# Kernel optimization log

Measured on AMD Instinct MI355X. Metric: run time of the kernel, lower is better.

Reference implementation:

```python
import jax, jax.numpy as jnp
import numpy as np

C = 256      # d_model
H = 8        # nhead
DF = 1024    # dim_feedforward
LE = 2048    # ego tokens
LA = 2048    # other-agent tokens
N_MATCH = 1024


def setup_inputs() -> dict:
    key = jax.random.key(0)
    ks = jax.random.split(key, 16)
    def rn(k, shape, s=0.02):
        return jax.random.normal(k, shape, dtype=jnp.float32) * s
    inp = {}
    inp['x_ego'] = jax.random.normal(ks[0], (LE, C), dtype=jnp.float32)
    inp['x_agent'] = jax.random.normal(ks[1], (LA, C), dtype=jnp.float32)
    # query_fusion MLP(2C -> C -> C -> C), torch Linear weight is (out, in)
    inp['Wf1'] = rn(ks[2], (C, 2 * C)); inp['bf1'] = jnp.zeros((C,), jnp.float32)
    inp['Wf2'] = rn(ks[3], (C, C));     inp['bf2'] = jnp.zeros((C,), jnp.float32)
    inp['Wf3'] = rn(ks[4], (C, C));     inp['bf3'] = jnp.zeros((C,), jnp.float32)
    # nn.MultiheadAttention packed in-proj and out-proj
    inp['Wqkv'] = rn(ks[5], (3 * C, C)); inp['bqkv'] = jnp.zeros((3 * C,), jnp.float32)
    inp['Wo'] = rn(ks[6], (C, C));       inp['bo'] = jnp.zeros((C,), jnp.float32)
    # FFN
    inp['W1'] = rn(ks[7], (DF, C)); inp['b1'] = jnp.zeros((DF,), jnp.float32)
    inp['W2'] = rn(ks[8], (C, DF)); inp['b2'] = jnp.zeros((C,), jnp.float32)
    # LayerNorms
    inp['g1'] = jnp.ones((C,), jnp.float32); inp['be1'] = jnp.zeros((C,), jnp.float32)
    inp['g2'] = jnp.ones((C,), jnp.float32); inp['be2'] = jnp.zeros((C,), jnp.float32)
    # unique 1D positions: first N_MATCH agent positions overlap ego, rest don't
    inp['pos_ego'] = jnp.arange(LE, dtype=jnp.int32)
    pa = np.concatenate([np.arange(N_MATCH), np.arange(LA - N_MATCH) + 10_000_000])
    inp['pos_agent'] = jnp.asarray(pa, dtype=jnp.int32)
    inp['n_remain'] = LA - N_MATCH  # static python int
    return inp


def _ln(t, g, b):
    m = t.mean(-1, keepdims=True)
    v = t.var(-1, keepdims=True)
    return (t - m) / jnp.sqrt(v + 1e-5) * g + b


def reference(x_ego, x_agent, Wf1, bf1, Wf2, bf2, Wf3, bf3, Wqkv, bqkv, Wo, bo,
              W1, b1, W2, b2, g1, be1, g2, be2, pos_ego, pos_agent, n_remain):
    # ---- position-keyed grouping / fuse (replaces the host-side dict loop) ----
    eq = pos_agent[:, None] == pos_ego[None, :]          # [La, Le]
    matched_e = eq.any(axis=0)                           # ego token has same-pos agent token
    agent_for_ego = jnp.argmax(eq, axis=0)               # [Le] matching agent index (valid where matched)
    fused_in = jnp.concatenate([x_ego, x_agent[agent_for_ego]], axis=-1)  # [Le, 2C]
    h = jax.nn.relu(fused_in @ Wf1.T + bf1)
    h = jax.nn.relu(h @ Wf2.T + bf2)
    fused = h @ Wf3.T + bf3                              # query_fusion MLP output [Le, C]
    ego_out = jnp.where(matched_e[:, None], fused, x_ego)
    # agent tokens with no ego match, in original agent order (fixed count n_remain)
    remain_idx = jnp.nonzero(~eq.any(axis=1), size=n_remain)[0]
    q = jnp.concatenate([ego_out, x_agent[remain_idx]], axis=0)[None]  # (1, Lq, C)
    kv = jnp.concatenate([x_ego, x_agent], axis=0)[None]               # (1, Lk, C)
    # ---- MultiheadAttention (batch_first, eval: dropout off) ----
    Wq, Wk, Wv = jnp.split(Wqkv, 3, axis=0)
    bq, bk, bv = jnp.split(bqkv, 3, axis=0)
    dh = C // H
    def heads(t, W, b):
        return (t @ W.T + b).reshape(1, -1, H, dh).transpose(0, 2, 1, 3)
    qh, kh, vh = heads(q, Wq, bq), heads(kv, Wk, bk), heads(kv, Wv, bv)
    scores = jnp.einsum('bhqd,bhkd->bhqk', qh, kh) / (float(dh) ** 0.5)
    attn = jax.nn.softmax(scores, axis=-1)
    o = jnp.einsum('bhqk,bhkd->bhqd', attn, vh).transpose(0, 2, 1, 3).reshape(1, -1, C)
    o = o @ Wo.T + bo
    # ---- residual + norm1 + FFN + residual + norm2 ----
    yq = _ln(q + o, g1, be1)
    ff = jax.nn.relu(yq @ W1.T + b1) @ W2.T + b2
    return _ln(yq + ff, g2, be2)
```

## Files before the change

### kernel.cpp

```cpp
#include <hip/hip_runtime.h>


#define LE 2048
#define LA 2048
#define CDIM 256
#define HN 8
#define DH 32
#define DFF 1024
#define NREM 1024
#define LQC 3072
#define LKC 4096
#define KSPLIT 4
#define NIT (LKC / KSPLIT / 64)

typedef unsigned short u16;
typedef unsigned int u32;
typedef __attribute__((ext_vector_type(8))) short bf16x8;
typedef __attribute__((ext_vector_type(4))) float f32x4;

__device__ __forceinline__ u32 pk_bf16(float a, float b) {
    u32 ua = (__builtin_bit_cast(u32, a) + 0x8000u) >> 16;
    u32 ub = (__builtin_bit_cast(u32, b) + 0x8000u) >> 16;
    return ua | (ub << 16);
}
__device__ __forceinline__ u16 bf16_1(float a) {
    return (u16)((__builtin_bit_cast(u32, a) + 0x8000u) >> 16);
}
__device__ __forceinline__ float fast_exp2(float x) {
    return __builtin_amdgcn_exp2f(x);
}

__global__ __launch_bounds__(1024) void k_match(const int* __restrict__ pos_ego,
                                                const int* __restrict__ pos_agent,
                                                int* __restrict__ afe,
                                                int* __restrict__ matched,
                                                int* __restrict__ unmatched) {
    __shared__ int keyA[4096], valA[4096], keyE[4096];
    const int t = threadIdx.x;
#pragma unroll
    for (int i = 0; i < 4; ++i) { keyA[t + i * 1024] = -1; keyE[t + i * 1024] = -1; }
    __syncthreads();
#pragma unroll
    for (int i = 0; i < 2; ++i) {
        int a = t + i * 1024;
        int p = pos_agent[a];
        u32 h = ((u32)p * 2654435761u) >> 20;
        while (true) {
            int prev = atomicCAS(&keyA[h], -1, p);
            if (prev == -1) { valA[h] = a; break; }
            h = (h + 1) & 4095;
        }
        int e = t + i * 1024;
        int pe = pos_ego[e];
        u32 he = ((u32)pe * 2654435761u) >> 20;
        while (true) {
            int prev = atomicCAS(&keyE[he], -1, pe);
            if (prev == -1) break;
            he = (he + 1) & 4095;
        }
    }
    __syncthreads();
#pragma unroll
    for (int i = 0; i < 2; ++i) {
        int e = t + i * 1024;
        int p = pos_ego[e];
        u32 h = ((u32)p * 2654435761u) >> 20;
        int idx = 0, fnd = 0;
        while (true) {
            int k = keyA[h];
            if (k == p) { idx = valA[h]; fnd = 1; break; }
            if (k == -1) break;
            h = (h + 1) & 4095;
        }
        afe[e] = idx;
        matched[e] = fnd;
        int a = t + i * 1024;
        int pa_ = pos_agent[a];
        u32 ha = ((u32)pa_ * 2654435761u) >> 20;
        int fnd2 = 0;
        while (true) {
            int k = keyE[ha];
            if (k == pa_) { fnd2 = 1; break; }
            if (k == -1) break;
            ha = (ha + 1) & 4095;
        }
        unmatched[a] = !fnd2;
    }
}

__global__ __launch_bounds__(256) void k_prep(const float* __restrict__ x_ego,
                                              const float* __restrict__ x_agent,
                                              u16* __restrict__ kv_b) {
    int t = blockIdx.x * 256 + threadIdx.x;
    int j = t >> 5, c8 = t & 31;
    const float* src = (j < LE) ? (x_ego + (size_t)j * CDIM)
                                : (x_agent + (size_t)(j - LE) * CDIM);
    float4 f0 = *(const float4*)(src + c8 * 8);
    float4 f1 = *(const float4*)(src + c8 * 8 + 4);
    uint4 o;
    o.x = pk_bf16(f0.x, f0.y); o.y = pk_bf16(f0.z, f0.w);
    o.z = pk_bf16(f1.x, f1.y); o.w = pk_bf16(f1.z, f1.w);
    *(uint4*)(kv_b + (size_t)j * CDIM + c8 * 8) = o;
}

struct WPtrs { const float* p[7]; };
__constant__ __device__ const int woff[8] = {0, 131072, 196608, 262144,
                                             458752, 524288, 786432, 1048576};

__global__ __launch_bounds__(256) void k_stage2(const int* __restrict__ unmatched,
                                                int* __restrict__ remain,
                                                const int* __restrict__ afe,
                                                const float* __restrict__ x_ego,
                                                const float* __restrict__ x_agent,
                                                u16* __restrict__ fused_b,
                                                WPtrs wp, u16* __restrict__ wb) {
    int b = blockIdx.x;
    if (b == 0) {
        __shared__ int s[256];
        int t = threadIdx.x;
        int base_i = t * 8;
        int flags[8];
        int cnt = 0;
#pragma unroll
        for (int j = 0; j < 8; ++j) { flags[j] = unmatched[base_i + j]; cnt += flags[j]; }
        s[t] = cnt;
        __syncthreads();
        for (int off = 1; off < 256; off <<= 1) {
            int v = (t >= off) ? s[t - off] : 0;
            __syncthreads();
            s[t] += v;
            __syncthreads();
        }
        int pos = s[t] - cnt;
#pragma unroll
        for (int j = 0; j < 8; ++j) {
            if (flags[j]) {
                if (pos < NREM) remain[pos] = base_i + j;
                pos++;
            }
        }
    } else if (b <= 512) {
        int t = (b - 1) * 256 + threadIdx.x;
        int e = t >> 6, c8 = t & 63;
        const float* src;
        int col;
        if (c8 < 32) { src = x_ego + (size_t)e * CDIM; col = c8 * 8; }
        else { src = x_agent + (size_t)afe[e] * CDIM; col = (c8 - 32) * 8; }
        float4 f0 = *(const float4*)(src + col);
        float4 f1 = *(const float4*)(src + col + 4);
        uint4 o;
        o.x = pk_bf16(f0.x, f0.y); o.y = pk_bf16(f0.z, f0.w);
        o.z = pk_bf16(f1.x, f1.y); o.w = pk_bf16(f1.z, f1.w);
        *(uint4*)(fused_b + (size_t)e * 512 + c8 * 8) = o;
    } else {
        int g = ((b - 513) * 256 + threadIdx.x) * 8;
        int s = 0;
#pragma unroll
        for (int i = 1; i < 7; ++i) s += (g >= woff[i]);
        const float* src = wp.p[s] + (g - woff[s]);
        float4 f0 = *(const float4*)(src);
        float4 f1 = *(const float4*)(src + 4);
        uint4 o;
        o.x = pk_bf16(f0.x, f0.y); o.y = pk_bf16(f0.z, f0.w);
        o.z = pk_bf16(f1.x, f1.y); o.w = pk_bf16(f1.z, f1.w);
        *(uint4*)(wb + g) = o;
    }
}

__global__ __launch_bounds__(256) void k_finalize_q(const int* __restrict__ matched,
                                                    const int* __restrict__ remain,
                                                    const float* __restrict__ x_ego,
                                                    const float* __restrict__ x_agent,
                                                    float* __restrict__ qbuf,
                                                    u16* __restrict__ qbuf_b) {
    int t = blockIdx.x * 256 + threadIdx.x;
    int row = t >> 5, c8 = t & 31;
    const float* src;
    if (row < LE) {
        src = matched[row] ? (qbuf + (size_t)row * CDIM) : (x_ego + (size_t)row * CDIM);
    } else {
        int idx = remain[row - LE];
        idx = min(max(idx, 0), LA - 1);
        src = x_agent + (size_t)idx * CDIM;
    }
    float4 f0 = *(const float4*)(src + c8 * 8);
    float4 f1 = *(const float4*)(src + c8 * 8 + 4);
    float* dst = qbuf + (size_t)row * CDIM + c8 * 8;
    *(float4*)(dst) = f0;
    *(float4*)(dst + 4) = f1;
    uint4 o;
    o.x = pk_bf16(f0.x, f0.y); o.y = pk_bf16(f0.z, f0.w);
    o.z = pk_bf16(f1.x, f1.y); o.w = pk_bf16(f1.z, f1.w);
    *(uint4*)(qbuf_b + (size_t)row * CDIM + c8 * 8) = o;
}

template <int EPI, bool RELU>
__global__ __launch_bounds__(256) void gemm_bf16(const u16* __restrict__ A,
                                                 const u16* __restrict__ B,
                                                 const float* __restrict__ bias,
                                                 void* __restrict__ C,
                                                 int M, int N, int K) {
    const int tid = threadIdx.x;
    const int w = tid >> 6, lane = tid & 63;
    const int quad = lane >> 4, qi = lane & 15;
    const int wm = w >> 1, wn = w & 1;
    const int bm = blockIdx.y * 64, bn = blockIdx.x * 64;

    const u16* pa0 = A + (size_t)(bm + wm * 32 + qi) * K + quad * 8;
    const u16* pa1 = pa0 + (size_t)16 * K;
    const u16* pb0 = B + (size_t)(bn + wn * 32 + qi) * K + quad * 8;
    const u16* pb1 = pb0 + (size_t)16 * K;

    f32x4 acc00 = {0.f, 0.f, 0.f, 0.f}, acc01 = {0.f, 0.f, 0.f, 0.f};
    f32x4 acc10 = {0.f, 0.f, 0.f, 0.f}, acc11 = {0.f, 0.f, 0.f, 0.f};

#pragma unroll 4
    for (int k = 0; k < K; k += 32) {
        bf16x8 a0 = *(const bf16x8*)(pa0 + k);
        bf16x8 a1 = *(const bf16x8*)(pa1 + k);
        bf16x8 b0 = *(const bf16x8*)(pb0 + k);
        bf16x8 b1 = *(const bf16x8*)(pb1 + k);
        acc00 = __builtin_amdgcn_mfma_f32_16x16x32_bf16(a0, b0, acc00, 0, 0, 0);
        acc01 = __builtin_amdgcn_mfma_f32_16x16x32_bf16(a0, b1, acc01, 0, 0, 0);
        acc10 = __builtin_amdgcn_mfma_f32_16x16x32_bf16(a1, b0, acc10, 0, 0, 0);
        acc11 = __builtin_amdgcn_mfma_f32_16x16x32_bf16(a1, b1, acc11, 0, 0, 0);
    }

#pragma unroll
    for (int i = 0; i < 2; ++i) {
#pragma unroll
        for (int j = 0; j < 2; ++j) {
            f32x4 acc = (i == 0) ? (j == 0 ? acc00 : acc01) : (j == 0 ? acc10 : acc11);
            int n = bn + wn * 32 + j * 16 + qi;
            int mbase = bm + wm * 32 + i * 16 + quad * 4;
            float bs = bias[n];
            float v[4];
#pragma unroll
            for (int r = 0; r < 4; ++r) {
                float x = acc[r] + bs;
                if (RELU) x = fmaxf(x, 0.f);
                v[r] = x;
            }
            if (EPI == 0) {
                float* Cf = (float*)C;
#pragma unroll
                for (int r = 0; r < 4; ++r) Cf[(size_t)(mbase + r) * N + n] = v[r];
            } else {
                u16* Cb = (u16*)C;
#pragma unroll
                for (int r = 0; r < 4; ++r) Cb[(size_t)(mbase + r) * N + n] = bf16_1(v[r]);
            }
        }
    }
}

__global__ __launch_bounds__(256) void k_qkv(const u16* __restrict__ qbuf_b,
                                             const u16* __restrict__ kv_b,
                                             const u16* __restrict__ Wq,
                                             const u16* __restrict__ Wkv,
                                             const float* __restrict__ bqkv,
                                             u16* __restrict__ qb,
                                             u16* __restrict__ kbp,
                                             u16* __restrict__ vtb,
                                             float qscale) {
    int b = blockIdx.x;
    const u16 *A, *B;
    const float* bias;
    int bm, bn, mode;
    if (b < 192) {
        A = qbuf_b; B = Wq; bias = bqkv;
        bm = (b >> 2) * 64; bn = (b & 3) * 64; mode = 0;
    } else {
        int c = b - 192;
        A = kv_b; B = Wkv; bias = bqkv + 256;
        bm = (c >> 3) * 64; bn = (c & 7) * 64; mode = 1;
    }
    const int tid = threadIdx.x;
    const int w = tid >> 6, lane = tid & 63;
    const int quad = lane >> 4, qi = lane & 15;
    const int wm = w >> 1, wn = w & 1;
    const int K = 256;

    const u16* pa0 = A + (size_t)(bm + wm * 32 + qi) * K + quad * 8;
    const u16* pa1 = pa0 + (size_t)16 * K;
    const u16* pb0 = B + (size_t)(bn + wn * 32 + qi) * K + quad * 8;
    const u16* pb1 = pb0 + (size_t)16 * K;

    f32x4 acc00 = {0.f, 0.f, 0.f, 0.f}, acc01 = {0.f, 0.f, 0.f, 0.f};
    f32x4 acc10 = {0.f, 0.f, 0.f, 0.f}, acc11 = {0.f, 0.f, 0.f, 0.f};
#pragma unroll 4
    for (int k = 0; k < 256; k += 32) {
        bf16x8 a0 = *(const bf16x8*)(pa0 + k);
        bf16x8 a1 = *(const bf16x8*)(pa1 + k);
        bf16x8 b0 = *(const bf16x8*)(pb0 + k);
        bf16x8 b1 = *(const bf16x8*)(pb1 + k);
        acc00 = __builtin_amdgcn_mfma_f32_16x16x32_bf16(a0, b0, acc00, 0, 0, 0);
        acc01 = __builtin_amdgcn_mfma_f32_16x16x32_bf16(a0, b1, acc01, 0, 0, 0);
        acc10 = __builtin_amdgcn_mfma_f32_16x16x32_bf16(a1, b0, acc10, 0, 0, 0);
        acc11 = __builtin_amdgcn_mfma_f32_16x16x32_bf16(a1, b1, acc11, 0, 0, 0);
    }
#pragma unroll
    for (int i = 0; i < 2; ++i) {
#pragma unroll
        for (int j = 0; j < 2; ++j) {
            f32x4 acc = (i == 0) ? (j == 0 ? acc00 : acc01) : (j == 0 ? acc10 : acc11);
            int n = bn + wn * 32 + j * 16 + qi;
            int mbase = bm + wm * 32 + i * 16 + quad * 4;
            float bs = bias[n];
            float v[4];
#pragma unroll
            for (int r = 0; r < 4; ++r) v[r] = acc[r] + bs;
            if (mode == 0) {
#pragma unroll
                for (int r = 0; r < 4; ++r)
                    qb[(size_t)(mbase + r) * 256 + n] = bf16_1(v[r] * qscale);
            } else if (n < 256) {
#pragma unroll
                for (int r = 0; r < 4; ++r)
                    kbp[(size_t)(mbase + r) * 256 + n] = bf16_1(v[r]);
            } else {
                ushort4 o4;
                o4.x = bf16_1(v[0]); o4.y = bf16_1(v[1]);
                o4.z = bf16_1(v[2]); o4.w = bf16_1(v[3]);
                *(ushort4*)(vtb + (size_t)(n - 256) * LKC + mbase) = o4;
            }
        }
    }
}

__global__ __launch_bounds__(256) void attn_mfma(const u16* __restrict__ qb,
                                                 const u16* __restrict__ kb,
                                                 const u16* __restrict__ vtb,
                                                 float* __restrict__ Pl,
                                                 float* __restrict__ Pacc) {
    __shared__ u16 Kt[2][64 * 32];
    __shared__ u16 Vt[2][32 * 64];
    __shared__ u16 plds[4][16 * 64];
    const int tid = threadIdx.x;
    const int w = tid >> 6, lane = tid & 63;
    const int quad = lane >> 4, qi = lane & 15;
    const int h = blockIdx.y, ks = blockIdx.z;
    const int q0 = blockIdx.x * 64 + w * 16;

    bf16x8 qf = *(const bf16x8*)(qb + (size_t)(q0 + qi) * CDIM + h * DH + quad * 8);

    f32x4 O0 = {0.f, 0.f, 0.f, 0.f}, O1 = {0.f, 0.f, 0.f, 0.f};
    float lsum = 0.f;

    const int krow = w * 16 + (lane >> 2), kcp = lane & 3;
    const int kc = kcp ^ (krow & 3);
    const u16* kg0 = kb + (size_t)krow * CDIM + h * DH + kc * 8;
    const int kdst = krow * 32 + kcp * 8;
    const int vd = w * 8 + (lane >> 3), vcp = lane & 7;
    const int vc = vcp ^ (vd & 7);
    const u16* vg0 = vtb + (size_t)(h * DH + vd) * LKC + vc * 8;
    const int vdst = vd * 64 + vcp * 8;

    const int ka0 = qi * 32 + ((quad ^ (qi & 3)) << 3);
    const int v00o = qi * 64 + ((quad ^ (qi & 7)) << 3);
    const int v01o = qi * 64 + (((quad + 4) ^ (qi & 7)) << 3);
    const int swz = (qi & 7);
    const int rd0 = qi * 64 + ((quad ^ swz) << 3);
    const int rd1 = qi * 64 + (((4 + quad) ^ swz) << 3);
    const int half = (quad & 1) << 2;

    int kt = ks * (LKC / KSPLIT);
    {
        bf16x8 kr = *(const bf16x8*)(kg0 + (size_t)kt * CDIM);
        bf16x8 vr = *(const bf16x8*)(vg0 + kt);
        *(bf16x8*)&Kt[0][kdst] = kr;
        *(bf16x8*)&Vt[0][vdst] = vr;
    }
    int buf = 0;
    for (int it = 0; it < NIT; ++it, kt += 64) {
        __syncthreads();
        bf16x8 knext, vnext;
        const bool more = (it + 1 < NIT);
        if (more) {
            knext = *(const bf16x8*)(kg0 + (size_t)(kt + 64) * CDIM);
            vnext = *(const bf16x8*)(vg0 + kt + 64);
        }

        bf16x8 a0 = *(const bf16x8*)&Kt[buf][ka0];
        bf16x8 a1 = *(const bf16x8*)&Kt[buf][ka0 + 16 * 32];
        bf16x8 a2 = *(const bf16x8*)&Kt[buf][ka0 + 32 * 32];
        bf16x8 a3 = *(const bf16x8*)&Kt[buf][ka0 + 48 * 32];
        f32x4 z = {0.f, 0.f, 0.f, 0.f};
        f32x4 s0 = __builtin_amdgcn_mfma_f32_16x16x32_bf16(a0, qf, z, 0, 0, 0);
        f32x4 s1 = __builtin_amdgcn_mfma_f32_16x16x32_bf16(a1, qf, z, 0, 0, 0);
        f32x4 s2 = __builtin_amdgcn_mfma_f32_16x16x32_bf16(a2, qf, z, 0, 0, 0);
        f32x4 s3 = __builtin_amdgcn_mfma_f32_16x16x32_bf16(a3, qf, z, 0, 0, 0);

        float p0[4], p1[4], p2[4], p3[4];
#pragma unroll
        for (int r = 0; r < 4; ++r) {
            p0[r] = fast_exp2(s0[r]); p1[r] = fast_exp2(s1[r]);
            p2[r] = fast_exp2(s2[r]); p3[r] = fast_exp2(s3[r]);
            lsum += p0[r] + p1[r] + p2[r] + p3[r];
        }

        u16* pb = &plds[w][0];
#pragma unroll
        for (int t = 0; t < 4; ++t) {
            int jg = t * 2 + (quad >> 1);
            int off = qi * 64 + ((jg ^ swz) << 3) + half;
            uint2 pw;
            float* pp = (t == 0) ? p0 : (t == 1) ? p1 : (t == 2) ? p2 : p3;
            pw.x = pk_bf16(pp[0], pp[1]);
            pw.y = pk_bf16(pp[2], pp[3]);
            *(uint2*)&pb[off] = pw;
        }
        bf16x8 pa0 = *(bf16x8*)&pb[rd0];
        bf16x8 pa1 = *(bf16x8*)&pb[rd1];

        bf16x8 v00 = *(const bf16x8*)&Vt[buf][v00o];
        bf16x8 v01 = *(const bf16x8*)&Vt[buf][v01o];
        bf16x8 v10 = *(const bf16x8*)&Vt[buf][v00o + 16 * 64];
        bf16x8 v11 = *(const bf16x8*)&Vt[buf][v01o + 16 * 64];
        O0 = __builtin_amdgcn_mfma_f32_16x16x32_bf16(pa0, v00, O0, 0, 0, 0);
        O0 = __builtin_amdgcn_mfma_f32_16x16x32_bf16(pa1, v01, O0, 0, 0, 0);
        O1 = __builtin_amdgcn_mfma_f32_16x16x32_bf16(pa0, v10, O1, 0, 0, 0);
        O1 = __builtin_amdgcn_mfma_f32_16x16x32_bf16(pa1, v11, O1, 0, 0, 0);

        if (more) {
            *(bf16x8*)&Kt[buf ^ 1][kdst] = knext;
            *(bf16x8*)&Vt[buf ^ 1][vdst] = vnext;
        }
        buf ^= 1;
    }

    lsum += __shfl_xor(lsum, 16, 64);
    lsum += __shfl_xor(lsum, 32, 64);

    int pbase = (h * KSPLIT + ks) * LQC + q0;
    if (quad == 0) Pl[pbase + qi] = lsum;
#pragma unroll
    for (int r = 0; r < 4; ++r) {
        int q = quad * 4 + r;
        float* pa = Pacc + (size_t)(pbase + q) * 32;
        pa[qi] = O0[r];
        pa[16 + qi] = O1[r];
    }
}

__global__ __launch_bounds__(256) void attn_combine(const float* __restrict__ Pl,
                                                    const float* __restrict__ Pacc,
                                                    u16* __restrict__ attn_b) {
    int t = blockIdx.x * 256 + threadIdx.x;
    int row = t >> 6;
    int h = (t >> 3) & 7;
    int d4 = t & 7;
    float L = 0.f;
    float o[4] = {};
#pragma unroll
    for (int ck = 0; ck < KSPLIT; ++ck) {
        size_t pidx = (size_t)(h * KSPLIT + ck) * LQC + row;
        L += Pl[pidx];
        float4 a = *(const float4*)(Pacc + pidx * 32 + d4 * 4);
        o[0] += a.x; o[1] += a.y; o[2] += a.z; o[3] += a.w;
    }
    float inv = 1.0f / L;
    ushort4 ov;
    ov.x = bf16_1(o[0] * inv); ov.y = bf16_1(o[1] * inv);
    ov.z = bf16_1(o[2] * inv); ov.w = bf16_1(o[3] * inv);
    *(ushort4*)(attn_b + (size_t)row * CDIM + h * DH + d4 * 4) = ov;
}

template <bool EMIT_BF16>
__global__ __launch_bounds__(256) void ln_kernel(const float* __restrict__ X,
                                                 const float* __restrict__ R,
                                                 const float* __restrict__ g,
                                                 const float* __restrict__ b,
                                                 float* __restrict__ out,
                                                 u16* __restrict__ out_b) {
    int lane = threadIdx.x & 63;
    int row = blockIdx.x * 4 + (threadIdx.x >> 6);
    const float* x = X + (size_t)row * CDIM;
    const float* r = R + (size_t)row * CDIM;
    float4 xv = *(const float4*)(x + lane * 4);
    float4 rv = *(const float4*)(r + lane * 4);
    float v[4] = {xv.x + rv.x, xv.y + rv.y, xv.z + rv.z, xv.w + rv.w};
    float s = v[0] + v[1] + v[2] + v[3];
    float sq = v[0] * v[0] + v[1] * v[1] + v[2] * v[2] + v[3] * v[3];
#pragma unroll
    for (int off = 32; off >= 1; off >>= 1) {
        s += __shfl_xor(s, off, 64);
        sq += __shfl_xor(sq, off, 64);
    }
    float mean = s * (1.f / 256.f);
    float var = sq * (1.f / 256.f) - mean * mean;
    float rstd = rsqrtf(var + 1e-5f);
    float4 gv = *(const float4*)(g + lane * 4);
    float4 bv = *(const float4*)(b + lane * 4);
    float4 o = make_float4((v[0] - mean) * rstd * gv.x + bv.x,
                           (v[1] - mean) * rstd * gv.y + bv.y,
                           (v[2] - mean) * rstd * gv.z + bv.z,
                           (v[3] - mean) * rstd * gv.w + bv.w);
    *(float4*)(out + (size_t)row * CDIM + lane * 4) = o;
    if (EMIT_BF16) {
        uint2 ob;
        ob.x = pk_bf16(o.x, o.y);
        ob.y = pk_bf16(o.z, o.w);
        *(uint2*)(out_b + (size_t)row * CDIM + lane * 4) = ob;
    }
}

extern "C" void kernel_launch(void* const* d_in, const int* in_sizes, int n_in,
                              void* d_out, int out_size, void* d_ws, size_t ws_size,
                              hipStream_t stream) {
    const float* x_ego = (const float*)d_in[0];
    const float* x_agent = (const float*)d_in[1];
    const float* Wf1 = (const float*)d_in[2];
    const float* bf1 = (const float*)d_in[3];
    const float* Wf2 = (const float*)d_in[4];
    const float* bf2 = (const float*)d_in[5];
    const float* Wf3 = (const float*)d_in[6];
    const float* bf3 = (const float*)d_in[7];
    const float* Wqkv = (const float*)d_in[8];
    const float* bqkv = (const float*)d_in[9];
    const float* Wo = (const float*)d_in[10];
    const float* bo = (const float*)d_in[11];
    const float* W1 = (const float*)d_in[12];
    const float* b1 = (const float*)d_in[13];
    const float* W2 = (const float*)d_in[14];
    const float* b2 = (const float*)d_in[15];
    const float* g1 = (const float*)d_in[16];
    const float* be1 = (const float*)d_in[17];
    const float* g2 = (const float*)d_in[18];
    const float* be2 = (const float*)d_in[19];
    const int* pos_ego = (const int*)d_in[20];
    const int* pos_agent = (const int*)d_in[21];

    float* ws = (float*)d_ws;
    size_t o = 0;
    float* qbuf = ws + o; o += 786432;
    float* o2 = ws + o; o += 786432;
    float* yq = ws + o; o += 786432;
    float* ff2 = ws + o; o += 786432;
    float* Pl = ws + o; o += HN * KSPLIT * LQC;
    float* Pacc = ws + o; o += (size_t)HN * KSPLIT * LQC * 32;
    u16* wb = (u16*)(ws + o); o += 524288;
    u16* fused_b = (u16*)(ws + o); o += 524288;
    u16* h1_b = (u16*)(ws + o); o += 262144;
    u16* h2_b = (u16*)(ws + o); o += 262144;
    u16* qbuf_b = (u16*)(ws + o); o += 393216;
    u16* kv_b = (u16*)(ws + o); o += 524288;
    u16* qb = (u16*)(ws + o); o += 393216;
    u16* kb = (u16*)(ws + o); o += 524288;
    u16* vtb = (u16*)(ws + o); o += 524288;
    u16* attn_b = (u16*)(ws + o); o += 393216;
    u16* ff1_b = (u16*)(ws + o); o += 1572864;
    u16* yq_b = (u16*)(ws + o); o += 393216;
    int* afe = (int*)(ws + o);
    int* matched = afe + LE;
    int* unmatched = matched + LE;
    int* remain = unmatched + LA;

    const u16* Wf1_b = wb + 0;
    const u16* Wf2_b = wb + 131072;
    const u16* Wf3_b = wb + 196608;
    const u16* Wq_b = wb + 262144;
    const u16* Wkv_b = wb + 327680;
    const u16* Wo_b = wb + 458752;
    const u16* W1_b = wb + 524288;
    const u16* W2_b = wb + 786432;

    k_match<<<1, 1024, 0, stream>>>(pos_ego, pos_agent, afe, matched, unmatched);
    k_prep<<<(LKC * 32) / 256, 256, 0, stream>>>(x_ego, x_agent, kv_b);
    WPtrs wp;
    wp.p[0] = Wf1; wp.p[1] = Wf2; wp.p[2] = Wf3; wp.p[3] = Wqkv;
    wp.p[4] = Wo; wp.p[5] = W1; wp.p[6] = W2;
    k_stage2<<<1025, 256, 0, stream>>>(unmatched, remain, afe, x_ego, x_agent,
                                       fused_b, wp, wb);

    const float qscale = 0.17677669529663687f * 1.4426950408889634f;

    gemm_bf16<1, true><<<dim3(4, 32), 256, 0, stream>>>(fused_b, Wf1_b, bf1, h1_b,
                                                        LE, 256, 512);
    gemm_bf16<1, true><<<dim3(4, 32), 256, 0, stream>>>(h1_b, Wf2_b, bf2, h2_b,
                                                        LE, 256, 256);
    gemm_bf16<0, false><<<dim3(4, 32), 256, 0, stream>>>(h2_b, Wf3_b, bf3, qbuf,
                                                         LE, 256, 256);
    k_finalize_q<<<(LQC * 32) / 256, 256, 0, stream>>>(matched, remain, x_ego, x_agent,
                                                       qbuf, qbuf_b);

    k_qkv<<<704, 256, 0, stream>>>(qbuf_b, kv_b, Wq_b, Wkv_b, bqkv, qb, kb, vtb, qscale);

    attn_mfma<<<dim3(LQC / 64, HN, KSPLIT), 256, 0, stream>>>(qb, kb, vtb, Pl, Pacc);
    attn_combine<<<(LQC * 64) / 256, 256, 0, stream>>>(Pl, Pacc, attn_b);

    gemm_bf16<0, false><<<dim3(4, 48), 256, 0, stream>>>(attn_b, Wo_b, bo, o2,
                                                         LQC, 256, 256);
    ln_kernel<true><<<LQC / 4, 256, 0, stream>>>(qbuf, o2, g1, be1, yq, yq_b);

    gemm_bf16<1, true><<<dim3(16, 48), 256, 0, stream>>>(yq_b, W1_b, b1, ff1_b,
                                                         LQC, DFF, 256);
    gemm_bf16<0, false><<<dim3(4, 48), 256, 0, stream>>>(ff1_b, W2_b, b2, ff2,
                                                         LQC, 256, DFF);
    ln_kernel<false><<<LQC / 4, 256, 0, stream>>>(yq, ff2, g2, be2, (float*)d_out, nullptr);
}
```

Before: 220.2 us.

## Fuse bf16 conversion of weights and inputs into GEMM operand loads

Removes the separate prep/stage2/finalize kernels. GEMMs now read fp32 weights and activations directly and convert to bf16 in registers. The remain-index prefix scan moves into k_match, and the q finalize/copy is folded into the third MLP GEMM. This cuts launches and intermediate global round-trips, but doubles the bytes read for B operands in every GEMM and repeats the conversion across blocks.

```diff
diff --git a/kernel.cpp b/kernel.cpp
--- a/kernel.cpp
+++ b/kernel.cpp
@@ -29,13 +29,22 @@
 __device__ __forceinline__ float fast_exp2(float x) {
     return __builtin_amdgcn_exp2f(x);
 }
+__device__ __forceinline__ bf16x8 pk8(const float* p) {
+    float4 f0 = *(const float4*)p;
+    float4 f1 = *(const float4*)(p + 4);
+    union { u32 u[4]; bf16x8 v; } r;
+    r.u[0] = pk_bf16(f0.x, f0.y); r.u[1] = pk_bf16(f0.z, f0.w);
+    r.u[2] = pk_bf16(f1.x, f1.y); r.u[3] = pk_bf16(f1.z, f1.w);
+    return r.v;
+}
 
 __global__ __launch_bounds__(1024) void k_match(const int* __restrict__ pos_ego,
                                                 const int* __restrict__ pos_agent,
                                                 int* __restrict__ afe,
                                                 int* __restrict__ matched,
-                                                int* __restrict__ unmatched) {
+                                                int* __restrict__ remain) {
     __shared__ int keyA[4096], valA[4096], keyE[4096];
+    __shared__ int ssum[1024];
     const int t = threadIdx.x;
 #pragma unroll
     for (int i = 0; i < 4; ++i) { keyA[t + i * 1024] = -1; keyE[t + i * 1024] = -1; }
@@ -50,8 +59,7 @@
             if (prev == -1) { valA[h] = a; break; }
             h = (h + 1) & 4095;
         }
-        int e = t + i * 1024;
-        int pe = pos_ego[e];
+        int pe = pos_ego[a];
         u32 he = ((u32)pe * 2654435761u) >> 20;
         while (true) {
             int prev = atomicCAS(&keyE[he], -1, pe);
@@ -74,132 +82,42 @@
         }
         afe[e] = idx;
         matched[e] = fnd;
-        int a = t + i * 1024;
-        int pa_ = pos_agent[a];
-        u32 ha = ((u32)pa_ * 2654435761u) >> 20;
-        int fnd2 = 0;
+    }
+    int f[2];
+#pragma unroll
+    for (int i = 0; i < 2; ++i) {
+        int a = t * 2 + i;
+        int p = pos_agent[a];
+        u32 h = ((u32)p * 2654435761u) >> 20;
+        int fnd = 0;
         while (true) {
-            int k = keyE[ha];
-            if (k == pa_) { fnd2 = 1; break; }
+            int k = keyE[h];
+            if (k == p) { fnd = 1; break; }
             if (k == -1) break;
-            ha = (ha + 1) & 4095;
-        }
-        unmatched[a] = !fnd2;
-    }
-}
-
-__global__ __launch_bounds__(256) void k_prep(const float* __restrict__ x_ego,
-                                              const float* __restrict__ x_agent,
-                                              u16* __restrict__ kv_b) {
-    int t = blockIdx.x * 256 + threadIdx.x;
-    int j = t >> 5, c8 = t & 31;
-    const float* src = (j < LE) ? (x_ego + (size_t)j * CDIM)
-                                : (x_agent + (size_t)(j - LE) * CDIM);
-    float4 f0 = *(const float4*)(src + c8 * 8);
-    float4 f1 = *(const float4*)(src + c8 * 8 + 4);
-    uint4 o;
-    o.x = pk_bf16(f0.x, f0.y); o.y = pk_bf16(f0.z, f0.w);
-    o.z = pk_bf16(f1.x, f1.y); o.w = pk_bf16(f1.z, f1.w);
-    *(uint4*)(kv_b + (size_t)j * CDIM + c8 * 8) = o;
-}
-
-struct WPtrs { const float* p[7]; };
-__constant__ __device__ const int woff[8] = {0, 131072, 196608, 262144,
-                                             458752, 524288, 786432, 1048576};
-
-__global__ __launch_bounds__(256) void k_stage2(const int* __restrict__ unmatched,
-                                                int* __restrict__ remain,
-                                                const int* __restrict__ afe,
-                                                const float* __restrict__ x_ego,
-                                                const float* __restrict__ x_agent,
-                                                u16* __restrict__ fused_b,
-                                                WPtrs wp, u16* __restrict__ wb) {
-    int b = blockIdx.x;
-    if (b == 0) {
-        __shared__ int s[256];
-        int t = threadIdx.x;
-        int base_i = t * 8;
-        int flags[8];
-        int cnt = 0;
-#pragma unroll
-        for (int j = 0; j < 8; ++j) { flags[j] = unmatched[base_i + j]; cnt += flags[j]; }
-        s[t] = cnt;
+            h = (h + 1) & 4095;
+        }
+        f[i] = !fnd;
+    }
+    int cnt = f[0] + f[1];
+    ssum[t] = cnt;
+    __syncthreads();
+    for (int off = 1; off < 1024; off <<= 1) {
+        int v = (t >= off) ? ssum[t - off] : 0;
         __syncthreads();
-        for (int off = 1; off < 256; off <<= 1) {
-            int v = (t >= off) ? s[t - off] : 0;
-            __syncthreads();
-            s[t] += v;
-            __syncthreads();
-        }
-        int pos = s[t] - cnt;
-#pragma unroll
-        for (int j = 0; j < 8; ++j) {
-            if (flags[j]) {
-                if (pos < NREM) remain[pos] = base_i + j;
-                pos++;
-            }
-        }
-    } else if (b <= 512) {
-        int t = (b - 1) * 256 + threadIdx.x;
-        int e = t >> 6, c8 = t & 63;
-        const float* src;
-        int col;
-        if (c8 < 32) { src = x_ego + (size_t)e * CDIM; col = c8 * 8; }
-        else { src = x_agent + (size_t)afe[e] * CDIM; col = (c8 - 32) * 8; }
-        float4 f0 = *(const float4*)(src + col);
-        float4 f1 = *(const float4*)(src + col + 4);
-        uint4 o;
-        o.x = pk_bf16(f0.x, f0.y); o.y = pk_bf16(f0.z, f0.w);
-        o.z = pk_bf16(f1.x, f1.y); o.w = pk_bf16(f1.z, f1.w);
-        *(uint4*)(fused_b + (size_t)e * 512 + c8 * 8) = o;
-    } else {
-        int g = ((b - 513) * 256 + threadIdx.x) * 8;
-        int s = 0;
-#pragma unroll
-        for (int i = 1; i < 7; ++i) s += (g >= woff[i]);
-        const float* src = wp.p[s] + (g - woff[s]);
-        float4 f0 = *(const float4*)(src);
-        float4 f1 = *(const float4*)(src + 4);
-        uint4 o;
-        o.x = pk_bf16(f0.x, f0.y); o.y = pk_bf16(f0.z, f0.w);
-        o.z = pk_bf16(f1.x, f1.y); o.w = pk_bf16(f1.z, f1.w);
-        *(uint4*)(wb + g) = o;
-    }
-}
-
-__global__ __launch_bounds__(256) void k_finalize_q(const int* __restrict__ matched,
-                                                    const int* __restrict__ remain,
-                                                    const float* __restrict__ x_ego,
-                                                    const float* __restrict__ x_agent,
-                                                    float* __restrict__ qbuf,
-                                                    u16* __restrict__ qbuf_b) {
-    int t = blockIdx.x * 256 + threadIdx.x;
-    int row = t >> 5, c8 = t & 31;
-    const float* src;
-    if (row < LE) {
-        src = matched[row] ? (qbuf + (size_t)row * CDIM) : (x_ego + (size_t)row * CDIM);
-    } else {
-        int idx = remain[row - LE];
-        idx = min(max(idx, 0), LA - 1);
-        src = x_agent + (size_t)idx * CDIM;
-    }
-    float4 f0 = *(const float4*)(src + c8 * 8);
-    float4 f1 = *(const float4*)(src + c8 * 8 + 4);
-    float* dst = qbuf + (size_t)row * CDIM + c8 * 8;
-    *(float4*)(dst) = f0;
-    *(float4*)(dst + 4) = f1;
-    uint4 o;
-    o.x = pk_bf16(f0.x, f0.y); o.y = pk_bf16(f0.z, f0.w);
-    o.z = pk_bf16(f1.x, f1.y); o.w = pk_bf16(f1.z, f1.w);
-    *(uint4*)(qbuf_b + (size_t)row * CDIM + c8 * 8) = o;
+        ssum[t] += v;
+        __syncthreads();
+    }
+    int pos = ssum[t] - cnt;
+    if (f[0]) { if (pos < NREM) remain[pos] = t * 2; pos++; }
+    if (f[1]) { if (pos < NREM) remain[pos] = t * 2 + 1; }
 }
 
 template <int EPI, bool RELU>
-__global__ __launch_bounds__(256) void gemm_bf16(const u16* __restrict__ A,
-                                                 const u16* __restrict__ B,
-                                                 const float* __restrict__ bias,
-                                                 void* __restrict__ C,
-                                                 int M, int N, int K) {
+__global__ __launch_bounds__(256) void gemm_bw(const u16* __restrict__ A,
+                                               const float* __restrict__ B,
+                                               const float* __restrict__ bias,
+                                               void* __restrict__ C,
+                                               int M, int N, int K) {
     const int tid = threadIdx.x;
     const int w = tid >> 6, lane = tid & 63;
     const int quad = lane >> 4, qi = lane & 15;
@@ -208,8 +126,8 @@
 
     const u16* pa0 = A + (size_t)(bm + wm * 32 + qi) * K + quad * 8;
     const u16* pa1 = pa0 + (size_t)16 * K;
-    const u16* pb0 = B + (size_t)(bn + wn * 32 + qi) * K + quad * 8;
-    const u16* pb1 = pb0 + (size_t)16 * K;
+    const float* pb0 = B + (size_t)(bn + wn * 32 + qi) * K + quad * 8;
+    const float* pb1 = pb0 + (size_t)16 * K;
 
     f32x4 acc00 = {0.f, 0.f, 0.f, 0.f}, acc01 = {0.f, 0.f, 0.f, 0.f};
     f32x4 acc10 = {0.f, 0.f, 0.f, 0.f}, acc11 = {0.f, 0.f, 0.f, 0.f};
@@ -218,8 +136,8 @@
     for (int k = 0; k < K; k += 32) {
         bf16x8 a0 = *(const bf16x8*)(pa0 + k);
         bf16x8 a1 = *(const bf16x8*)(pa1 + k);
-        bf16x8 b0 = *(const bf16x8*)(pb0 + k);
-        bf16x8 b1 = *(const bf16x8*)(pb1 + k);
+        bf16x8 b0 = pk8(pb0 + k);
+        bf16x8 b1 = pk8(pb1 + k);
         acc00 = __builtin_amdgcn_mfma_f32_16x16x32_bf16(a0, b0, acc00, 0, 0, 0);
         acc01 = __builtin_amdgcn_mfma_f32_16x16x32_bf16(a0, b1, acc01, 0, 0, 0);
         acc10 = __builtin_amdgcn_mfma_f32_16x16x32_bf16(a1, b0, acc10, 0, 0, 0);
@@ -234,97 +152,237 @@
             int n = bn + wn * 32 + j * 16 + qi;
             int mbase = bm + wm * 32 + i * 16 + quad * 4;
             float bs = bias[n];
-            float v[4];
 #pragma unroll
             for (int r = 0; r < 4; ++r) {
                 float x = acc[r] + bs;
                 if (RELU) x = fmaxf(x, 0.f);
-                v[r] = x;
+                if (EPI == 0) ((float*)C)[(size_t)(mbase + r) * N + n] = x;
+                else ((u16*)C)[(size_t)(mbase + r) * N + n] = bf16_1(x);
             }
-            if (EPI == 0) {
-                float* Cf = (float*)C;
-#pragma unroll
-                for (int r = 0; r < 4; ++r) Cf[(size_t)(mbase + r) * N + n] = v[r];
-            } else {
-                u16* Cb = (u16*)C;
-#pragma unroll
-                for (int r = 0; r < 4; ++r) Cb[(size_t)(mbase + r) * N + n] = bf16_1(v[r]);
+        }
+    }
+}
+
+__global__ __launch_bounds__(256) void k_mlp1(const float* __restrict__ x_ego,
+                                              const float* __restrict__ x_agent,
+                                              const int* __restrict__ afe,
+                                              const float* __restrict__ Wf1,
+                                              const float* __restrict__ bf1,
+                                              u16* __restrict__ h1_b) {
+    const int tid = threadIdx.x;
+    const int w = tid >> 6, lane = tid & 63;
+    const int quad = lane >> 4, qi = lane & 15;
+    const int wm = w >> 1, wn = w & 1;
+    const int bm = blockIdx.y * 64, bn = blockIdx.x * 64;
+
+    int e0 = bm + wm * 32 + qi, e1 = e0 + 16;
+    const float* pe0 = x_ego + (size_t)e0 * CDIM + quad * 8;
+    const float* pe1 = x_ego + (size_t)e1 * CDIM + quad * 8;
+    const float* pg0 = x_agent + (size_t)afe[e0] * CDIM + quad * 8;
+    const float* pg1 = x_agent + (size_t)afe[e1] * CDIM + quad * 8;
+    const float* pb0 = Wf1 + (size_t)(bn + wn * 32 + qi) * 512 + quad * 8;
+    const float* pb1 = pb0 + (size_t)16 * 512;
+
+    f32x4 acc00 = {0.f, 0.f, 0.f, 0.f}, acc01 = {0.f, 0.f, 0.f, 0.f};
+    f32x4 acc10 = {0.f, 0.f, 0.f, 0.f}, acc11 = {0.f, 0.f, 0.f, 0.f};
+
+#pragma unroll 4
+    for (int k = 0; k < 256; k += 32) {
+        bf16x8 a0 = pk8(pe0 + k);
+        bf16x8 a1 = pk8(pe1 + k);
+        bf16x8 b0 = pk8(pb0 + k);
+        bf16x8 b1 = pk8(pb1 + k);
+        acc00 = __builtin_amdgcn_mfma_f32_16x16x32_bf16(a0, b0, acc00, 0, 0, 0);
+        acc01 = __builtin_amdgcn_mfma_f32_16x16x32_bf16(a0, b1, acc01, 0, 0, 0);
+        acc10 = __builtin_amdgcn_mfma_f32_16x16x32_bf16(a1, b0, acc10, 0, 0, 0);
+        acc11 = __builtin_amdgcn_mfma_f32_16x16x32_bf16(a1, b1, acc11, 0, 0, 0);
+    }
+#pragma unroll 4
+    for (int k = 0; k < 256; k += 32) {
+        bf16x8 a0 = pk8(pg0 + k);
+        bf16x8 a1 = pk8(pg1 + k);
+        bf16x8 b0 = pk8(pb0 + 256 + k);
+        bf16x8 b1 = pk8(pb1 + 256 + k);
+        acc00 = __builtin_amdgcn_mfma_f32_16x16x32_bf16(a0, b0, acc00, 0, 0, 0);
+        acc01 = __builtin_amdgcn_mfma_f32_16x16x32_bf16(a0, b1, acc01, 0, 0, 0);
+        acc10 = __builtin_amdgcn_mfma_f32_16x16x32_bf16(a1, b0, acc10, 0, 0, 0);
+        acc11 = __builtin_amdgcn_mfma_f32_16x16x32_bf16(a1, b1, acc11, 0, 0, 0);
+    }
+
+#pragma unroll
+    for (int i = 0; i < 2; ++i) {
+#pragma unroll
+        for (int j = 0; j < 2; ++j) {
+            f32x4 acc = (i == 0) ? (j == 0 ? acc00 : acc01) : (j == 0 ? acc10 : acc11);
+            int n = bn + wn * 32 + j * 16 + qi;
+            int mbase = bm + wm * 32 + i * 16 + quad * 4;
+            float bs = bf1[n];
+#pragma unroll
+            for (int r = 0; r < 4; ++r)
+                h1_b[(size_t)(mbase + r) * 256 + n] = bf16_1(fmaxf(acc[r] + bs, 0.f));
+        }
+    }
+}
+
+__global__ __launch_bounds__(256) void k_mlp3f(const u16* __restrict__ h2_b,
+                                               const float* __restrict__ Wf3,
+                                               const float* __restrict__ bf3,
+                                               const int* __restrict__ matched,
+                                               const int* __restrict__ remain,
+                                               const float* __restrict__ x_ego,
+                                               const float* __restrict__ x_agent,
+                                               float* __restrict__ qbuf,
+                                               u16* __restrict__ qbuf_b) {
+    const int tid = threadIdx.x;
+    const int bm = blockIdx.y * 64, bn = blockIdx.x * 64;
+    if (bm >= LE) {
+        int row = bm + (tid >> 2);
+        int col = bn + (tid & 3) * 16;
+        int idx = remain[row - LE];
+        idx = min(max(idx, 0), LA - 1);
+        const float* src = x_agent + (size_t)idx * CDIM + col;
+        float* dq = qbuf + (size_t)row * CDIM + col;
+        u16* db = qbuf_b + (size_t)row * CDIM + col;
+#pragma unroll
+        for (int i = 0; i < 4; ++i) {
+            float4 v = *(const float4*)(src + i * 4);
+            *(float4*)(dq + i * 4) = v;
+            u32 p0 = pk_bf16(v.x, v.y), p1 = pk_bf16(v.z, v.w);
+            *(uint2*)(db + i * 4) = make_uint2(p0, p1);
+        }
+        return;
+    }
+    const int w = tid >> 6, lane = tid & 63;
+    const int quad = lane >> 4, qi = lane & 15;
+    const int wm = w >> 1, wn = w & 1;
+
+    const u16* pa0 = h2_b + (size_t)(bm + wm * 32 + qi) * 256 + quad * 8;
+    const u16* pa1 = pa0 + (size_t)16 * 256;
+    const float* pb0 = Wf3 + (size_t)(bn + wn * 32 + qi) * 256 + quad * 8;
+    const float* pb1 = pb0 + (size_t)16 * 256;
+
+    f32x4 acc00 = {0.f, 0.f, 0.f, 0.f}, acc01 = {0.f, 0.f, 0.f, 0.f};
+    f32x4 acc10 = {0.f, 0.f, 0.f, 0.f}, acc11 = {0.f, 0.f, 0.f, 0.f};
+#pragma unroll 4
+    for (int k = 0; k < 256; k += 32) {
+        bf16x8 a0 = *(const bf16x8*)(pa0 + k);
+        bf16x8 a1 = *(const bf16x8*)(pa1 + k);
+        bf16x8 b0 = pk8(pb0 + k);
+        bf16x8 b1 = pk8(pb1 + k);
+        acc00 = __builtin_amdgcn_mfma_f32_16x16x32_bf16(a0, b0, acc00, 0, 0, 0);
+        acc01 = __builtin_amdgcn_mfma_f32_16x16x32_bf16(a0, b1, acc01, 0, 0, 0);
+        acc10 = __builtin_amdgcn_mfma_f32_16x16x32_bf16(a1, b0, acc10, 0, 0, 0);
+        acc11 = __builtin_amdgcn_mfma_f32_16x16x32_bf16(a1, b1, acc11, 0, 0, 0);
+    }
+#pragma unroll
+    for (int i = 0; i < 2; ++i) {
+#pragma unroll
+        for (int j = 0; j < 2; ++j) {
+            f32x4 acc = (i == 0) ? (j == 0 ? acc00 : acc01) : (j == 0 ? acc10 : acc11);
+            int n = bn + wn * 32 + j * 16 + qi;
+            int mbase = bm + wm * 32 + i * 16 + quad * 4;
+            float bs = bf3[n];
+#pragma unroll
+            for (int r = 0; r < 4; ++r) {
+                int row = mbase + r;
+                float v = acc[r] + bs;
+                if (!matched[row]) v = x_ego[(size_t)row * CDIM + n];
+                qbuf[(size_t)row * CDIM + n] = v;
+                qbuf_b[(size_t)row * CDIM + n] = bf16_1(v);
             }
         }
     }
 }
 
 __global__ __launch_bounds__(256) void k_qkv(const u16* __restrict__ qbuf_b,
-                                             const u16* __restrict__ kv_b,
-                                             const u16* __restrict__ Wq,
-                                             const u16* __restrict__ Wkv,
+                                             const float* __restrict__ x_ego,
+                                             const float* __restrict__ x_agent,
+                                             const float* __restrict__ Wqkv,
                                              const float* __restrict__ bqkv,
                                              u16* __restrict__ qb,
                                              u16* __restrict__ kbp,
                                              u16* __restrict__ vtb,
                                              float qscale) {
     int b = blockIdx.x;
-    const u16 *A, *B;
-    const float* bias;
-    int bm, bn, mode;
-    if (b < 192) {
-        A = qbuf_b; B = Wq; bias = bqkv;
-        bm = (b >> 2) * 64; bn = (b & 3) * 64; mode = 0;
-    } else {
-        int c = b - 192;
-        A = kv_b; B = Wkv; bias = bqkv + 256;
-        bm = (c >> 3) * 64; bn = (c & 7) * 64; mode = 1;
-    }
     const int tid = threadIdx.x;
     const int w = tid >> 6, lane = tid & 63;
     const int quad = lane >> 4, qi = lane & 15;
     const int wm = w >> 1, wn = w & 1;
-    const int K = 256;
-
-    const u16* pa0 = A + (size_t)(bm + wm * 32 + qi) * K + quad * 8;
-    const u16* pa1 = pa0 + (size_t)16 * K;
-    const u16* pb0 = B + (size_t)(bn + wn * 32 + qi) * K + quad * 8;
-    const u16* pb1 = pb0 + (size_t)16 * K;
 
     f32x4 acc00 = {0.f, 0.f, 0.f, 0.f}, acc01 = {0.f, 0.f, 0.f, 0.f};
     f32x4 acc10 = {0.f, 0.f, 0.f, 0.f}, acc11 = {0.f, 0.f, 0.f, 0.f};
+
+    if (b < 192) {
+        const int bm = (b >> 2) * 64, bn = (b & 3) * 64;
+        const u16* pa0 = qbuf_b + (size_t)(bm + wm * 32 + qi) * 256 + quad * 8;
+        const u16* pa1 = pa0 + (size_t)16 * 256;
+        const float* pb0 = Wqkv + (size_t)(bn + wn * 32 + qi) * 256 + quad * 8;
+        const float* pb1 = pb0 + (size_t)16 * 256;
 #pragma unroll 4
-    for (int k = 0; k < 256; k += 32) {
-        bf16x8 a0 = *(const bf16x8*)(pa0 + k);
-        bf16x8 a1 = *(const bf16x8*)(pa1 + k);
-        bf16x8 b0 = *(const bf16x8*)(pb0 + k);
-        bf16x8 b1 = *(const bf16x8*)(pb1 + k);
-        acc00 = __builtin_amdgcn_mfma_f32_16x16x32_bf16(a0, b0, acc00, 0, 0, 0);
-        acc01 = __builtin_amdgcn_mfma_f32_16x16x32_bf16(a0, b1, acc01, 0, 0, 0);
-        acc10 = __builtin_amdgcn_mfma_f32_16x16x32_bf16(a1, b0, acc10, 0, 0, 0);
-        acc11 = __builtin_amdgcn_mfma_f32_16x16x32_bf16(a1, b1, acc11, 0, 0, 0);
-    }
-#pragma unroll
-    for (int i = 0; i < 2; ++i) {
-#pragma unroll
-        for (int j = 0; j < 2; ++j) {
-            f32x4 acc = (i == 0) ? (j == 0 ? acc00 : acc01) : (j == 0 ? acc10 : acc11);
-            int n = bn + wn * 32 + j * 16 + qi;
-            int mbase = bm + wm * 32 + i * 16 + quad * 4;
-            float bs = bias[n];
-            float v[4];
-#pragma unroll
-            for (int r = 0; r < 4; ++r) v[r] = acc[r] + bs;
-            if (mode == 0) {
+        for (int k = 0; k < 256; k += 32) {
+            bf16x8 a0 = *(const bf16x8*)(pa0 + k);
+            bf16x8 a1 = *(const bf16x8*)(pa1 + k);
+            bf16x8 b0 = pk8(pb0 + k);
+            bf16x8 b1 = pk8(pb1 + k);
+            acc00 = __builtin_amdgcn_mfma_f32_16x16x32_bf16(a0, b0, acc00, 0, 0, 0);
+            acc01 = __builtin_amdgcn_mfma_f32_16x16x32_bf16(a0, b1, acc01, 0, 0, 0);
+            acc10 = __builtin_amdgcn_mfma_f32_16x16x32_bf16(a1, b0, acc10, 0, 0, 0);
+            acc11 = __builtin_amdgcn_mfma_f32_16x16x32_bf16(a1, b1, acc11, 0, 0, 0);
+        }
+#pragma unroll
+        for (int i = 0; i < 2; ++i)
+#pragma unroll
+            for (int j = 0; j < 2; ++j) {
+                f32x4 acc = (i == 0) ? (j == 0 ? acc00 : acc01) : (j == 0 ? acc10 : acc11);
+                int n = bn + wn * 32 + j * 16 + qi;
+                int mbase = bm + wm * 32 + i * 16 + quad * 4;
+                float bs = bqkv[n];
 #pragma unroll
                 for (int r = 0; r < 4; ++r)
-                    qb[(size_t)(mbase + r) * 256 + n] = bf16_1(v[r] * qscale);
-            } else if (n < 256) {
-#pragma unroll
-                for (int r = 0; r < 4; ++r)
-                    kbp[(size_t)(mbase + r) * 256 + n] = bf16_1(v[r]);
-            } else {
-                ushort4 o4;
-                o4.x = bf16_1(v[0]); o4.y = bf16_1(v[1]);
-                o4.z = bf16_1(v[2]); o4.w = bf16_1(v[3]);
-                *(ushort4*)(vtb + (size_t)(n - 256) * LKC + mbase) = o4;
+                    qb[(size_t)(mbase + r) * 256 + n] = bf16_1((acc[r] + bs) * qscale);
             }
-        }
+    } else {
+        int c = b - 192;
+        const int bm = (c >> 3) * 64, bn = (c & 7) * 64;
+        int j0 = bm + wm * 32 + qi, j1 = j0 + 16;
+        const float* base = (bm < LE) ? x_ego : (x_agent - (size_t)LE * CDIM);
+        const float* pa0 = base + (size_t)j0 * CDIM + quad * 8;
+        const float* pa1 = base + (size_t)j1 * CDIM + quad * 8;
+        const float* pb0 = Wqkv + (size_t)(256 + bn + wn * 32 + qi) * 256 + quad * 8;
+        const float* pb1 = pb0 + (size_t)16 * 256;
+#pragma unroll 4
+        for (int k = 0; k < 256; k += 32) {
+            bf16x8 a0 = pk8(pa0 + k);
+            bf16x8 a1 = pk8(pa1 + k);
+            bf16x8 b0 = pk8(pb0 + k);
+            bf16x8 b1 = pk8(pb1 + k);
+            acc00 = __builtin_amdgcn_mfma_f32_16x16x32_bf16(a0, b0, acc00, 0, 0, 0);
+            acc01 = __builtin_amdgcn_mfma_f32_16x16x32_bf16(a0, b1, acc01, 0, 0, 0);
+            acc10 = __builtin_amdgcn_mfma_f32_16x16x32_bf16(a1, b0, acc10, 0, 0, 0);
+            acc11 = __builtin_amdgcn_mfma_f32_16x16x32_bf16(a1, b1, acc11, 0, 0, 0);
+        }
+#pragma unroll
+        for (int i = 0; i < 2; ++i)
+#pragma unroll
+            for (int j = 0; j < 2; ++j) {
+                f32x4 acc = (i == 0) ? (j == 0 ? acc00 : acc01) : (j == 0 ? acc10 : acc11);
+                int n = bn + wn * 32 + j * 16 + qi;
+                int mbase = bm + wm * 32 + i * 16 + quad * 4;
+                float bs = bqkv[256 + n];
+                float v[4];
+#pragma unroll
+                for (int r = 0; r < 4; ++r) v[r] = acc[r] + bs;
+                if (n < 256) {
+#pragma unroll
+                    for (int r = 0; r < 4; ++r)
+                        kbp[(size_t)(mbase + r) * 256 + n] = bf16_1(v[r]);
+                } else {
+                    ushort4 o4;
+                    o4.x = bf16_1(v[0]); o4.y = bf16_1(v[1]);
+                    o4.z = bf16_1(v[2]); o4.w = bf16_1(v[3]);
+                    *(ushort4*)(vtb + (size_t)(n - 256) * LKC + mbase) = o4;
+                }
+            }
     }
 }
 
@@ -539,12 +597,9 @@
     float* ff2 = ws + o; o += 786432;
     float* Pl = ws + o; o += HN * KSPLIT * LQC;
     float* Pacc = ws + o; o += (size_t)HN * KSPLIT * LQC * 32;
-    u16* wb = (u16*)(ws + o); o += 524288;
-    u16* fused_b = (u16*)(ws + o); o += 524288;
     u16* h1_b = (u16*)(ws + o); o += 262144;
     u16* h2_b = (u16*)(ws + o); o += 262144;
     u16* qbuf_b = (u16*)(ws + o); o += 393216;
-    u16* kv_b = (u16*)(ws + o); o += 524288;
     u16* qb = (u16*)(ws + o); o += 393216;
     u16* kb = (u16*)(ws + o); o += 524288;
     u16* vtb = (u16*)(ws + o); o += 524288;
@@ -553,49 +608,26 @@
     u16* yq_b = (u16*)(ws + o); o += 393216;
     int* afe = (int*)(ws + o);
     int* matched = afe + LE;
-    int* unmatched = matched + LE;
-    int* remain = unmatched + LA;
-
-    const u16* Wf1_b = wb + 0;
-    const u16* Wf2_b = wb + 131072;
-    const u16* Wf3_b = wb + 196608;
-    const u16* Wq_b = wb + 262144;
-    const u16* Wkv_b = wb + 327680;
-    const u16* Wo_b = wb + 458752;
-    const u16* W1_b = wb + 524288;
-    const u16* W2_b = wb + 786432;
-
-    k_match<<<1, 1024, 0, stream>>>(pos_ego, pos_agent, afe, matched, unmatched);
-    k_prep<<<(LKC * 32) / 256, 256, 0, stream>>>(x_ego, x_agent, kv_b);
-    WPtrs wp;
-    wp.p[0] = Wf1; wp.p[1] = Wf2; wp.p[2] = Wf3; wp.p[3] = Wqkv;
-    wp.p[4] = Wo; wp.p[5] = W1; wp.p[6] = W2;
-    k_stage2<<<1025, 256, 0, stream>>>(unmatched, remain, afe, x_ego, x_agent,
-                                       fused_b, wp, wb);
+    int* remain = matched + LE;
 
     const float qscale = 0.17677669529663687f * 1.4426950408889634f;
 
-    gemm_bf16<1, true><<<dim3(4, 32), 256, 0, stream>>>(fused_b, Wf1_b, bf1, h1_b,
-                                                        LE, 256, 512);
-    gemm_bf16<1, true><<<dim3(4, 32), 256, 0, stream>>>(h1_b, Wf2_b, bf2, h2_b,
-                                                        LE, 256, 256);
-    gemm_bf16<0, false><<<dim3(4, 32), 256, 0, stream>>>(h2_b, Wf3_b, bf3, qbuf,
-                                                         LE, 256, 256);
-    k_finalize_q<<<(LQC * 32) / 256, 256, 0, stream>>>(matched, remain, x_ego, x_agent,
-                                                       qbuf, qbuf_b);
-
-    k_qkv<<<704, 256, 0, stream>>>(qbuf_b, kv_b, Wq_b, Wkv_b, bqkv, qb, kb, vtb, qscale);
+    k_match<<<1, 1024, 0, stream>>>(pos_ego, pos_agent, afe, matched, remain);
+
+    k_mlp1<<<dim3(4, 32), 256, 0, stream>>>(x_ego, x_agent, afe, Wf1, bf1, h1_b);
+    gemm_bw<1, true><<<dim3(4, 32), 256, 0, stream>>>(h1_b, Wf2, bf2, h2_b, LE, 256, 256);
+    k_mlp3f<<<dim3(4, 48), 256, 0, stream>>>(h2_b, Wf3, bf3, matched, remain,
+                                             x_ego, x_agent, qbuf, qbuf_b);
+
+    k_qkv<<<704, 256, 0, stream>>>(qbuf_b, x_ego, x_agent, Wqkv, bqkv, qb, kb, vtb, qscale);
 
     attn_mfma<<<dim3(LQC / 64, HN, KSPLIT), 256, 0, stream>>>(qb, kb, vtb, Pl, Pacc);
     attn_combine<<<(LQC * 64) / 256, 256, 0, stream>>>(Pl, Pacc, attn_b);
 
-    gemm_bf16<0, false><<<dim3(4, 48), 256, 0, stream>>>(attn_b, Wo_b, bo, o2,
-                                                         LQC, 256, 256);
+    gemm_bw<0, false><<<dim3(4, 48), 256, 0, stream>>>(attn_b, Wo, bo, o2, LQC, 256, 256);
     ln_kernel<true><<<LQC / 4, 256, 0, stream>>>(qbuf, o2, g1, be1, yq, yq_b);
 
-    gemm_bf16<1, true><<<dim3(16, 48), 256, 0, stream>>>(yq_b, W1_b, b1, ff1_b,
-                                                         LQC, DFF, 256);
-    gemm_bf16<0, false><<<dim3(4, 48), 256, 0, stream>>>(ff1_b, W2_b, b2, ff2,
-                                                         LQC, 256, DFF);
+    gemm_bw<1, true><<<dim3(16, 48), 256, 0, stream>>>(yq_b, W1, b1, ff1_b, LQC, DFF, 256);
+    gemm_bw<0, false><<<dim3(4, 48), 256, 0, stream>>>(ff1_b, W2, b2, ff2, LQC, 256, DFF);
     ln_kernel<false><<<LQC / 4, 256, 0, stream>>>(yq, ff2, g2, be2, (float*)d_out, nullptr);
 }
```

New measurement: 247.7 us. +12.5%, slower.
